# Optimization experiments

Hardware: AMD Instinct MI355X
Metric: run time of the kernel (lower is better)

Reference implementation:

```python
import jax, jax.numpy as jnp
import numpy as np

EPS = 1e-5

def setup_inputs() -> dict:
    key = jax.random.key(0)
    kx, kw = jax.random.split(key)
    x = jax.random.normal(kx, (4, 2048, 4096), dtype=jnp.float32)
    W = jax.random.normal(kw, (4096, 4096), dtype=jnp.float32) * 0.02
    return {"x": x, "W": W}

def reference(x, W):
    # scale = mean absolute weight
    scale = jnp.mean(jnp.abs(W))
    Wn = W / (scale + EPS)
    # straight-through ternary rounding: forward = round(Wn), grad = identity
    Wq = Wn + jax.lax.stop_gradient(jnp.round(Wn) - Wn)
    # y = x @ Wq^T, then rescale by mean(|W|)
    y = jnp.einsum('bsi,oi->bso', x, Wq)
    return y * scale
```

## Files before the change

### kernel.cpp

```cpp
#include <hip/hip_runtime.h>


#define K_DIM 4096
#define N_DIM 4096
#define NKT   64

typedef __bf16 bf16x8 __attribute__((ext_vector_type(8)));
typedef float floatx4 __attribute__((ext_vector_type(4)));

__device__ __forceinline__ unsigned short f32_to_bf16(float f) {
    unsigned int u = __float_as_uint(f);
    u += 0x7fffu + ((u >> 16) & 1u);
    return (unsigned short)(u >> 16);
}

__global__ void reduce_abs_p1(const float4* __restrict__ W, double* __restrict__ partials, int n4) {
    int tid = blockIdx.x * blockDim.x + threadIdx.x;
    int stride = gridDim.x * blockDim.x;
    float s = 0.f;
    for (int i = tid; i < n4; i += stride) {
        float4 v = W[i];
        s += fabsf(v.x) + fabsf(v.y) + fabsf(v.z) + fabsf(v.w);
    }
    double d = (double)s;
#pragma unroll
    for (int o = 32; o > 0; o >>= 1) d += __shfl_down(d, o, 64);
    __shared__ double lds[4];
    if ((threadIdx.x & 63) == 0) lds[threadIdx.x >> 6] = d;
    __syncthreads();
    if (threadIdx.x == 0)
        partials[blockIdx.x] = lds[0] + lds[1] + lds[2] + lds[3];
}

__global__ void reduce_abs_p2(const double* __restrict__ partials, double* __restrict__ out) {
    double d = 0.0;
#pragma unroll
    for (int i = 0; i < 4; ++i) d += partials[threadIdx.x + i * 256];
#pragma unroll
    for (int o = 32; o > 0; o >>= 1) d += __shfl_down(d, o, 64);
    __shared__ double lds[4];
    if ((threadIdx.x & 63) == 0) lds[threadIdx.x >> 6] = d;
    __syncthreads();
    if (threadIdx.x == 0) *out = lds[0] + lds[1] + lds[2] + lds[3];
}

__global__ void prep(const float4* __restrict__ W, const float4* __restrict__ X,
                     const double* __restrict__ sum,
                     ushort4* __restrict__ Wq, ushort4* __restrict__ Xb,
                     int nW4, int nX4, double inv_cnt) {
    float scale = (float)(*sum * inv_cnt);
    float d = scale + 1e-5f;
    int tid = blockIdx.x * blockDim.x + threadIdx.x;
    int stride = gridDim.x * blockDim.x;
    for (int i = tid; i < nW4; i += stride) {
        float4 v = W[i];
        ushort4 q;
        q.x = f32_to_bf16(rintf(v.x / d));
        q.y = f32_to_bf16(rintf(v.y / d));
        q.z = f32_to_bf16(rintf(v.z / d));
        q.w = f32_to_bf16(rintf(v.w / d));
        Wq[i] = q;
    }
    for (int i = tid; i < nX4; i += stride) {
        float4 v = X[i];
        ushort4 q;
        q.x = f32_to_bf16(v.x);
        q.y = f32_to_bf16(v.y);
        q.z = f32_to_bf16(v.z);
        q.w = f32_to_bf16(v.w);
        Xb[i] = q;
    }
}

__global__ __launch_bounds__(512, 2) void gemm_bt(
    const unsigned short* __restrict__ A, const unsigned short* __restrict__ B,
    float* __restrict__ C, const double* __restrict__ sum, double inv_cnt) {

    __shared__ __attribute__((aligned(16))) unsigned short As[2][2][128 * 64];
    __shared__ __attribute__((aligned(16))) unsigned short Bs[2][2][128 * 64];

    const int tid  = threadIdx.x;
    const int w    = tid >> 6;
    const int lane = tid & 63;
    const int wm   = w >> 2;
    const int wn   = w & 3;

    const int bid = blockIdx.y * gridDim.x + blockIdx.x;
    const int swz = (bid & 7) * 64 + (bid >> 3);
    const size_t m0 = (size_t)(swz >> 4) * 256;
    const size_t n0 = (size_t)(swz & 15) * 256;

    const int srow   = lane >> 3;
    const int schunk = (lane & 7) ^ srow;
    const unsigned short* pA = A + (m0 + (size_t)(w * 8 + srow)) * K_DIM + schunk * 8;
    const unsigned short* pB = B + (n0 + (size_t)(w * 8 + srow)) * K_DIM + schunk * 8;

    const int fm    = lane & 15;
    const int q     = lane >> 4;
    const int cs0   = (q ^ (fm & 7)) * 8;
    const int cs1   = ((4 + q) ^ (fm & 7)) * 8;
    const int abase = fm * 64;
    const int bh    = wn >> 1;
    const int bbase = (wn & 1) * 4096 + fm * 64;

    floatx4 acc[8][4] = {};
    bf16x8  afr[2][4];
    bf16x8  bfr[2][2][2];

#define STAGE_A(bb, h, kt) do {                                                            \
        __builtin_amdgcn_global_load_lds(                                                  \
            (const __attribute__((address_space(1))) void*)(pA + ((h) * 128 + 0) * K_DIM + (kt) * 64), \
            (__attribute__((address_space(3))) void*)&As[bb][h][w * 512 + 0], 16, 0, 0);   \
        __builtin_amdgcn_global_load_lds(                                                  \
            (const __attribute__((address_space(1))) void*)(pA + ((h) * 128 + 64) * K_DIM + (kt) * 64), \
            (__attribute__((address_space(3))) void*)&As[bb][h][w * 512 + 4096], 16, 0, 0); \
    } while (0)

#define STAGE_B(bb, h, kt) do {                                                            \
        __builtin_amdgcn_global_load_lds(                                                  \
            (const __attribute__((address_space(1))) void*)(pB + ((h) * 128 + 0) * K_DIM + (kt) * 64), \
            (__attribute__((address_space(3))) void*)&Bs[bb][h][w * 512 + 0], 16, 0, 0);   \
        __builtin_amdgcn_global_load_lds(                                                  \
            (const __attribute__((address_space(1))) void*)(pB + ((h) * 128 + 64) * K_DIM + (kt) * 64), \
            (__attribute__((address_space(3))) void*)&Bs[bb][h][w * 512 + 4096], 16, 0, 0); \
    } while (0)

#define READ_A(b, mh) do {                                                                 \
        _Pragma("unroll")                                                                  \
        for (int t = 0; t < 4; ++t) {                                                      \
            afr[0][t] = *(const bf16x8*)&As[b][wm][((mh) * 4 + t) * 1024 + abase + cs0];   \
            afr[1][t] = *(const bf16x8*)&As[b][wm][((mh) * 4 + t) * 1024 + abase + cs1];   \
        }                                                                                  \
    } while (0)

#define READ_B(b, nh) do {                                                                 \
        _Pragma("unroll")                                                                  \
        for (int u = 0; u < 2; ++u) {                                                      \
            bfr[nh][0][u] = *(const bf16x8*)&Bs[b][bh][bbase + ((nh) * 2 + u) * 1024 + cs0]; \
            bfr[nh][1][u] = *(const bf16x8*)&Bs[b][bh][bbase + ((nh) * 2 + u) * 1024 + cs1]; \
        }                                                                                  \
    } while (0)

#define MFMA16(mh, nh) do {                                                                \
        _Pragma("unroll")                                                                  \
        for (int t = 0; t < 4; ++t)                                                        \
            _Pragma("unroll")                                                              \
            for (int u = 0; u < 2; ++u) {                                                  \
                acc[(mh) * 4 + t][(nh) * 2 + u] = __builtin_amdgcn_mfma_f32_16x16x32_bf16( \
                    afr[0][t], bfr[nh][0][u], acc[(mh) * 4 + t][(nh) * 2 + u], 0, 0, 0);   \
                acc[(mh) * 4 + t][(nh) * 2 + u] = __builtin_amdgcn_mfma_f32_16x16x32_bf16( \
                    afr[1][t], bfr[nh][1][u], acc[(mh) * 4 + t][(nh) * 2 + u], 0, 0, 0);   \
            }                                                                              \
    } while (0)

#define KTILE(b, j, DOA, DOB, VMW) do {                                                    \
                                                                              \
        READ_A(b, 0);                                                                      \
        READ_B(b, 0);                                                                      \
        if (DOA) STAGE_A((b) ^ 1, 0, (j) + 1);                                             \
        asm volatile("s_waitcnt lgkmcnt(8)" ::: "memory");                                 \
        __builtin_amdgcn_s_barrier();                                                      \
        asm volatile("s_waitcnt lgkmcnt(0)" ::: "memory");                                 \
        __builtin_amdgcn_s_setprio(1);                                                     \
        MFMA16(0, 0);                                                                      \
        __builtin_amdgcn_s_setprio(0);                                                     \
        __builtin_amdgcn_s_barrier();                                                      \
                                                                              \
        READ_B(b, 1);                                                                      \
        if (DOA) STAGE_A((b) ^ 1, 1, (j) + 1);                                             \
        __builtin_amdgcn_s_barrier();                                                      \
        asm volatile("s_waitcnt lgkmcnt(0)" ::: "memory");                                 \
        __builtin_amdgcn_s_setprio(1);                                                     \
        MFMA16(0, 1);                                                                      \
        __builtin_amdgcn_s_setprio(0);                                                     \
        __builtin_amdgcn_s_barrier();                                                      \
                                                                              \
        READ_A(b, 1);                                                                      \
        if (DOB) STAGE_B(b, 0, (j) + 2);                                                   \
        __builtin_amdgcn_s_barrier();                                                      \
        asm volatile("s_waitcnt lgkmcnt(0)" ::: "memory");                                 \
        __builtin_amdgcn_s_setprio(1);                                                     \
        MFMA16(1, 0);                                                                      \
        __builtin_amdgcn_s_setprio(0);                                                     \
        __builtin_amdgcn_s_barrier();                                                      \
                                                                              \
        if (DOB) STAGE_B(b, 1, (j) + 2);                                                   \
        __builtin_amdgcn_s_barrier();                                                      \
        __builtin_amdgcn_s_setprio(1);                                                     \
        MFMA16(1, 1);                                                                      \
        __builtin_amdgcn_s_setprio(0);                                                     \
        asm volatile(VMW ::: "memory");                                                    \
        __builtin_amdgcn_s_barrier();                                                      \
    } while (0)

    STAGE_B(0, 0, 0); STAGE_B(0, 1, 0);
    STAGE_A(0, 0, 0); STAGE_A(0, 1, 0);
    STAGE_B(1, 0, 1); STAGE_B(1, 1, 1);
    asm volatile("s_waitcnt vmcnt(4)" ::: "memory");
    __builtin_amdgcn_s_barrier();

    for (int j = 0; j < NKT - 2; j += 2) {
        KTILE(0, j,     1, 1, "s_waitcnt vmcnt(4)");
        KTILE(1, j + 1, 1, 1, "s_waitcnt vmcnt(4)");
    }
    KTILE(0, NKT - 2, 1, 0, "s_waitcnt vmcnt(0)");
    KTILE(1, NKT - 1, 0, 0, "");

#undef KTILE
#undef MFMA16
#undef READ_B
#undef READ_A
#undef STAGE_B
#undef STAGE_A

    const float scale = (float)(*sum * inv_cnt);
    const size_t m0c = m0 + (size_t)wm * 128;
    const size_t n0c = n0 + (size_t)wn * 64;
#pragma unroll
    for (int mf = 0; mf < 8; ++mf) {
#pragma unroll
        for (int nf = 0; nf < 4; ++nf) {
            float* cp = C + (m0c + mf * 16 + q * 4) * N_DIM + n0c + nf * 16 + fm;
#pragma unroll
            for (int r = 0; r < 4; ++r)
                cp[(size_t)r * N_DIM] = acc[mf][nf][r] * scale;
        }
    }
}

extern "C" void kernel_launch(void* const* d_in, const int* in_sizes, int n_in,
                              void* d_out, int out_size, void* d_ws, size_t ws_size,
                              hipStream_t stream) {
    const float* x = (const float*)d_in[0];
    const float* W = (const float*)d_in[1];
    float* y = (float*)d_out;

    const int nW = in_sizes[1];
    const int M  = in_sizes[0] / K_DIM;

    double* d_sum = (double*)d_ws;
    double* d_partials = (double*)((char*)d_ws + 16);
    unsigned short* xb = (unsigned short*)((char*)d_ws + 16 + 1024 * sizeof(double));
    unsigned short* wq = xb + (size_t)M * K_DIM;
    const double inv_cnt = 1.0 / (double)nW;

    reduce_abs_p1<<<1024, 256, 0, stream>>>((const float4*)W, d_partials, nW / 4);
    reduce_abs_p2<<<1, 256, 0, stream>>>(d_partials, d_sum);
    prep<<<2048, 256, 0, stream>>>((const float4*)W, (const float4*)x, d_sum,
                                   (ushort4*)wq, (ushort4*)xb,
                                   nW / 4, in_sizes[0] / 4, inv_cnt);

    dim3 grid(N_DIM / 256, M / 256);
    gemm_bt<<<grid, 512, 0, stream>>>(xb, wq, y, d_sum, inv_cnt);
}
```

Baseline: 570.1 us.

## Software-pipeline LDS fragment reads across MFMA phases with double-buffered registers

```diff
diff --git a/kernel.cpp b/kernel.cpp
--- a/kernel.cpp
+++ b/kernel.cpp
@@ -104,8 +104,10 @@
     const int bbase = (wn & 1) * 4096 + fm * 64;
 
     floatx4 acc[8][4] = {};
-    bf16x8  afr[2][4];
-    bf16x8  bfr[2][2][2];
+    bf16x8 a0[2][4];
+    bf16x8 a1[2][4];
+    bf16x8 b0v[2][2];
+    bf16x8 b1v[2][2];
 
 #define STAGE_A(bb, h, kt) do {                                                            \
         __builtin_amdgcn_global_load_lds(                                                  \
@@ -125,71 +127,66 @@
             (__attribute__((address_space(3))) void*)&Bs[bb][h][w * 512 + 4096], 16, 0, 0); \
     } while (0)
 
-#define READ_A(b, mh) do {                                                                 \
+#define READ_A_HALF(dst, b, mh) do {                                                       \
         _Pragma("unroll")                                                                  \
         for (int t = 0; t < 4; ++t) {                                                      \
-            afr[0][t] = *(const bf16x8*)&As[b][wm][((mh) * 4 + t) * 1024 + abase + cs0];   \
-            afr[1][t] = *(const bf16x8*)&As[b][wm][((mh) * 4 + t) * 1024 + abase + cs1];   \
+            dst[0][t] = *(const bf16x8*)&As[b][wm][((mh) * 4 + t) * 1024 + abase + cs0];   \
+            dst[1][t] = *(const bf16x8*)&As[b][wm][((mh) * 4 + t) * 1024 + abase + cs1];   \
         }                                                                                  \
     } while (0)
 
-#define READ_B(b, nh) do {                                                                 \
+#define READ_B_HALF(dst, b, nh) do {                                                       \
         _Pragma("unroll")                                                                  \
         for (int u = 0; u < 2; ++u) {                                                      \
-            bfr[nh][0][u] = *(const bf16x8*)&Bs[b][bh][bbase + ((nh) * 2 + u) * 1024 + cs0]; \
-            bfr[nh][1][u] = *(const bf16x8*)&Bs[b][bh][bbase + ((nh) * 2 + u) * 1024 + cs1]; \
+            dst[0][u] = *(const bf16x8*)&Bs[b][bh][bbase + ((nh) * 2 + u) * 1024 + cs0];   \
+            dst[1][u] = *(const bf16x8*)&Bs[b][bh][bbase + ((nh) * 2 + u) * 1024 + cs1];   \
         }                                                                                  \
     } while (0)
 
-#define MFMA16(mh, nh) do {                                                                \
+#define MFMA16(mh, nh, Af, Bf) do {                                                        \
         _Pragma("unroll")                                                                  \
         for (int t = 0; t < 4; ++t)                                                        \
             _Pragma("unroll")                                                              \
             for (int u = 0; u < 2; ++u) {                                                  \
                 acc[(mh) * 4 + t][(nh) * 2 + u] = __builtin_amdgcn_mfma_f32_16x16x32_bf16( \
-                    afr[0][t], bfr[nh][0][u], acc[(mh) * 4 + t][(nh) * 2 + u], 0, 0, 0);   \
+                    Af[0][t], Bf[0][u], acc[(mh) * 4 + t][(nh) * 2 + u], 0, 0, 0);         \
                 acc[(mh) * 4 + t][(nh) * 2 + u] = __builtin_amdgcn_mfma_f32_16x16x32_bf16( \
-                    afr[1][t], bfr[nh][1][u], acc[(mh) * 4 + t][(nh) * 2 + u], 0, 0, 0);   \
+                    Af[1][t], Bf[1][u], acc[(mh) * 4 + t][(nh) * 2 + u], 0, 0, 0);         \
             }                                                                              \
     } while (0)
 
-#define KTILE(b, j, DOA, DOB, VMW) do {                                                    \
-                                                                              \
-        READ_A(b, 0);                                                                      \
-        READ_B(b, 0);                                                                      \
+#define KTILE(b, j, DOA, DOB, PF, VM1S, VM2S) do {                                         \
+                             \
         if (DOA) STAGE_A((b) ^ 1, 0, (j) + 1);                                             \
-        asm volatile("s_waitcnt lgkmcnt(8)" ::: "memory");                                 \
-        __builtin_amdgcn_s_barrier();                                                      \
+        READ_B_HALF(b1v, b, 1);                                                            \
+        __builtin_amdgcn_s_setprio(1);                                                     \
+        MFMA16(0, 0, a0, b0v);                                                             \
+        __builtin_amdgcn_s_setprio(0);                                                     \
         asm volatile("s_waitcnt lgkmcnt(0)" ::: "memory");                                 \
-        __builtin_amdgcn_s_setprio(1);                                                     \
-        MFMA16(0, 0);                                                                      \
-        __builtin_amdgcn_s_setprio(0);                                                     \
-        __builtin_amdgcn_s_barrier();                                                      \
-                                                                              \
-        READ_B(b, 1);                                                                      \
+        __builtin_amdgcn_s_barrier();                                                      \
+                              \
         if (DOA) STAGE_A((b) ^ 1, 1, (j) + 1);                                             \
-        __builtin_amdgcn_s_barrier();                                                      \
+        READ_A_HALF(a1, b, 1);                                                             \
+        __builtin_amdgcn_s_setprio(1);                                                     \
+        MFMA16(0, 1, a0, b1v);                                                             \
+        __builtin_amdgcn_s_setprio(0);                                                     \
+        asm volatile(VM1S ::: "memory");                                                   \
+        __builtin_amdgcn_s_barrier();                                                      \
+                        \
+        if (DOB) STAGE_B(b, 0, (j) + 2);                                                   \
+        __builtin_amdgcn_s_setprio(1);                                                     \
+        MFMA16(1, 0, a1, b0v);                                                             \
+        __builtin_amdgcn_s_setprio(0);                                                     \
+        if (PF) READ_B_HALF(b0v, (b) ^ 1, 0);                                              \
+        asm volatile(VM2S ::: "memory");                                                   \
+        __builtin_amdgcn_s_barrier();                                                      \
+                        \
+        if (DOB) STAGE_B(b, 1, (j) + 2);                                                   \
+        if (PF) READ_A_HALF(a0, (b) ^ 1, 0);                                               \
+        __builtin_amdgcn_s_setprio(1);                                                     \
+        MFMA16(1, 1, a1, b1v);                                                             \
+        __builtin_amdgcn_s_setprio(0);                                                     \
         asm volatile("s_waitcnt lgkmcnt(0)" ::: "memory");                                 \
-        __builtin_amdgcn_s_setprio(1);                                                     \
-        MFMA16(0, 1);                                                                      \
-        __builtin_amdgcn_s_setprio(0);                                                     \
-        __builtin_amdgcn_s_barrier();                                                      \
-                                                                              \
-        READ_A(b, 1);                                                                      \
-        if (DOB) STAGE_B(b, 0, (j) + 2);                                                   \
-        __builtin_amdgcn_s_barrier();                                                      \
-        asm volatile("s_waitcnt lgkmcnt(0)" ::: "memory");                                 \
-        __builtin_amdgcn_s_setprio(1);                                                     \
-        MFMA16(1, 0);                                                                      \
-        __builtin_amdgcn_s_setprio(0);                                                     \
-        __builtin_amdgcn_s_barrier();                                                      \
-                                                                              \
-        if (DOB) STAGE_B(b, 1, (j) + 2);                                                   \
-        __builtin_amdgcn_s_barrier();                                                      \
-        __builtin_amdgcn_s_setprio(1);                                                     \
-        MFMA16(1, 1);                                                                      \
-        __builtin_amdgcn_s_setprio(0);                                                     \
-        asm volatile(VMW ::: "memory");                                                    \
         __builtin_amdgcn_s_barrier();                                                      \
     } while (0)
 
@@ -198,18 +195,20 @@
     STAGE_B(1, 0, 1); STAGE_B(1, 1, 1);
     asm volatile("s_waitcnt vmcnt(4)" ::: "memory");
     __builtin_amdgcn_s_barrier();
+    READ_A_HALF(a0, 0, 0);
+    READ_B_HALF(b0v, 0, 0);
 
     for (int j = 0; j < NKT - 2; j += 2) {
-        KTILE(0, j,     1, 1, "s_waitcnt vmcnt(4)");
-        KTILE(1, j + 1, 1, 1, "s_waitcnt vmcnt(4)");
-    }
-    KTILE(0, NKT - 2, 1, 0, "s_waitcnt vmcnt(0)");
-    KTILE(1, NKT - 1, 0, 0, "");
+        KTILE(0, j,     1, (j < NKT - 2), 1, "s_waitcnt vmcnt(4)", "s_waitcnt vmcnt(2)");
+        KTILE(1, j + 1, 1, (j + 1 < NKT - 2), 1, "s_waitcnt vmcnt(4)", "s_waitcnt vmcnt(2)");
+    }
+    KTILE(0, NKT - 2, 1, 0, 1, "s_waitcnt vmcnt(4)", "s_waitcnt vmcnt(0)");
+    KTILE(1, NKT - 1, 0, 0, 0, "", "");
 
 #undef KTILE
 #undef MFMA16
-#undef READ_B
-#undef READ_A
+#undef READ_B_HALF
+#undef READ_A_HALF
 #undef STAGE_B
 #undef STAGE_A
 
```

Result: slower. 588.6 us (+3.2%).
